# Performance work log

Measured on AMD Instinct MI355X. Metric: run time of the kernel, lower is better.

Reference implementation:

```python
import jax, jax.numpy as jnp
import numpy as np

B, S, HID = 1, 2048, 4096
NH, NKV, D = 32, 8, 128          # query heads, kv heads, head_dim
GROUPS = NH // NKV               # GQA repeat factor = 4
WINDOW = 1024                    # sliding-window size
ROPE_BASE = 10000.0


def setup_inputs() -> dict:
    key = jax.random.key(0)
    k = jax.random.split(key, 5)
    hidden_states = jax.random.normal(k[0], (B, S, HID), jnp.float32)
    Wq = jax.random.normal(k[1], (HID, HID), jnp.float32) * 0.02
    Wk = jax.random.normal(k[2], (NKV * D, HID), jnp.float32) * 0.02
    Wv = jax.random.normal(k[3], (NKV * D, HID), jnp.float32) * 0.02
    Wo = jax.random.normal(k[4], (HID, HID), jnp.float32) * 0.02
    position_ids = jnp.arange(S, dtype=jnp.int64 if jax.config.jax_enable_x64 else jnp.int32)[None, :]
    # Sliding-window causal additive mask [B,1,S,S]: key j visible to query i iff i-WINDOW < j <= i
    i = jnp.arange(S)
    visible = (i[None, :] <= i[:, None]) & (i[:, None] - i[None, :] < WINDOW)
    neg = jnp.finfo(jnp.float32).min
    attention_mask = jnp.where(visible, 0.0, neg)[None, None, :, :].astype(jnp.float32)
    return {"hidden_states": hidden_states, "attention_mask": attention_mask,
            "position_ids": position_ids, "Wq": Wq, "Wk": Wk, "Wv": Wv, "Wo": Wo}


def _rotate_half(x):
    x1, x2 = x[..., : D // 2], x[..., D // 2:]
    return jnp.concatenate((-x2, x1), axis=-1)


def _rope_cos_sin(position_ids, dtype):
    # inv_freq over even dims; gather-by-position_ids == direct indexing
    inv_freq = 1.0 / (ROPE_BASE ** (jnp.arange(0, D, 2, dtype=jnp.float32) / D))  # [D/2]
    freqs = position_ids.astype(jnp.float32)[..., None] * inv_freq                # [B,S,D/2]
    emb = jnp.concatenate((freqs, freqs), axis=-1)                                # [B,S,D]
    cos = jnp.cos(emb)[:, None, :, :].astype(dtype)                               # [B,1,S,D]
    sin = jnp.sin(emb)[:, None, :, :].astype(dtype)
    return cos, sin


def reference(hidden_states, attention_mask, position_ids, Wq, Wk, Wv, Wo):
    bsz, q_len, _ = hidden_states.shape
    # projections (nn.Linear: y = x @ W.T)
    q = (hidden_states @ Wq.T).reshape(bsz, q_len, NH, D).transpose(0, 2, 1, 3)    # [B,NH,S,D]
    k = (hidden_states @ Wk.T).reshape(bsz, q_len, NKV, D).transpose(0, 2, 1, 3)   # [B,NKV,S,D]
    v = (hidden_states @ Wv.T).reshape(bsz, q_len, NKV, D).transpose(0, 2, 1, 3)
    cos, sin = _rope_cos_sin(position_ids, q.dtype)
    q = q * cos + _rotate_half(q) * sin
    k = k * cos + _rotate_half(k) * sin
    # GQA repeat_kv (repeat_interleave along head dim)
    k = jnp.repeat(k, GROUPS, axis=1)                                              # [B,NH,S,D]
    v = jnp.repeat(v, GROUPS, axis=1)
    scores = jnp.einsum('bhqd,bhkd->bhqk', q, k) / np.sqrt(D)                       # [B,NH,S,S]
    scores = scores + attention_mask
    scores = jnp.maximum(scores, jnp.finfo(scores.dtype).min)
    probs = jax.nn.softmax(scores.astype(jnp.float32), axis=-1).astype(q.dtype)
    out = jnp.einsum('bhqk,bhkd->bhqd', probs, v)                                   # [B,NH,S,D]
    out = out.transpose(0, 2, 1, 3).reshape(bsz, q_len, HID)
    return out @ Wo.T
```

## Files before the change

### kernel.cpp

```cpp
#include <hip/hip_runtime.h>

#define S_LEN 2048
#define HID   4096
#define NH    32
#define NKV   8
#define DH    128
#define KVD   (NKV*DH)
#define WIN   1024
#define NTOT  6144

typedef __bf16 bf16_t;
typedef __bf16 bfrag  __attribute__((ext_vector_type(8)));
typedef __bf16 bf4    __attribute__((ext_vector_type(4)));
typedef float  ffrag  __attribute__((ext_vector_type(4)));
typedef float  f4     __attribute__((ext_vector_type(4)));

__global__ __launch_bounds__(256) void f32_to_bf16_kernel(const float* __restrict__ src,
                                                          bf16_t* __restrict__ dst, int n4) {
  int i = blockIdx.x * 256 + threadIdx.x;
  if (i < n4) {
    ffrag v = *(const ffrag*)(src + (size_t)i * 4);
    bf4 o;
    o[0] = (bf16_t)v[0]; o[1] = (bf16_t)v[1]; o[2] = (bf16_t)v[2]; o[3] = (bf16_t)v[3];
    *(bf4*)(dst + (size_t)i * 4) = o;
  }
}

__global__ __launch_bounds__(256) void cvt4_kernel(const float* __restrict__ h,
    const float* __restrict__ Wq, const float* __restrict__ Wk, const float* __restrict__ Wv,
    bf16_t* __restrict__ hB, bf16_t* __restrict__ WqB,
    bf16_t* __restrict__ WkB, bf16_t* __restrict__ WvB) {
  int i = blockIdx.x * 256 + threadIdx.x;
  const int N0 = S_LEN * HID / 4;
  const int N1 = N0 + HID * HID / 4;
  const int N2 = N1 + KVD * HID / 4;
  const float* s; bf16_t* d; int off;
  if (i < N0)      { s = h;  d = hB;  off = i; }
  else if (i < N1) { s = Wq; d = WqB; off = i - N0; }
  else if (i < N2) { s = Wk; d = WkB; off = i - N1; }
  else             { s = Wv; d = WvB; off = i - N2; }
  ffrag v = *(const ffrag*)(s + (size_t)off * 4);
  bf4 o;
  o[0] = (bf16_t)v[0]; o[1] = (bf16_t)v[1]; o[2] = (bf16_t)v[2]; o[3] = (bf16_t)v[3];
  *(bf4*)(d + (size_t)off * 4) = o;
}


__device__ __forceinline__ void load_lds16(const bf16_t* g, bf16_t* l) {
  __builtin_amdgcn_global_load_lds((__attribute__((address_space(1))) void*)g,
                                   (__attribute__((address_space(3))) void*)l,
                                   16, 0, 0);
}

#define BARW() asm volatile("s_barrier" ::: "memory")
#define WAITV(n) asm volatile("s_waitcnt vmcnt(" #n ")" ::: "memory")

template <int BNR, int OUT_MODE>
__device__ __forceinline__ void gemm_body(const bf16_t* __restrict__ A,
                                          const bf16_t* __restrict__ B,
                                          void* __restrict__ Cv,
                                          int N, bf16_t* lds) {
  constexpr int K     = 4096;
  constexpr int NT    = K / 32;
  constexpr int NTF   = BNR / 64;
  constexpr int WCOLS = BNR / 4;
  constexpr int ABUFE = 4096;
  constexpr int BBUFE = BNR * 32;

  bf16_t* Asb = lds;
  bf16_t* Bsb = lds + 4 * ABUFE;

  const int raw  = blockIdx.x;
  const int xcd  = raw & 7;
  const int slot = raw >> 3;
  const int bx   = xcd * 4 + (slot & 3);
  const int by   = slot >> 2;
  const int row0 = by * 128;
  const int col0 = bx * BNR;

  const int tid  = threadIdx.x;
  const int wave = tid >> 6;
  const int lane = tid & 63;
  const int wr = wave >> 2, wc = wave & 3;
  const int n = lane & 15, qd = lane >> 4;

  const int rsub = tid >> 2;
  const int sg   = (tid & 3) ^ (rsub & 3);
  const bf16_t* Ag  = A + (size_t)(row0 + rsub) * K + sg * 8;
  const bf16_t* Bg  = B + (size_t)(col0 + rsub) * K + sg * 8;
  const bf16_t* Bg2 = B + (size_t)(col0 + 128 + rsub) * K + sg * 8;
  const int wbase = wave * 512;

  const int lsw = n * 32 + (qd ^ (n & 3)) * 8;

  ffrag acc[4][NTF];
#pragma unroll
  for (int mt = 0; mt < 4; ++mt)
#pragma unroll
    for (int nt = 0; nt < NTF; ++nt) {
      acc[mt][nt][0] = 0.f; acc[mt][nt][1] = 0.f; acc[mt][nt][2] = 0.f; acc[mt][nt][3] = 0.f;
    }

  auto STAGE = [&](int t, int b) {
    const int ko = t * 32;
    load_lds16(Ag + ko, Asb + b * ABUFE + wbase);
    load_lds16(Bg + ko, Bsb + b * BBUFE + wbase);
    if constexpr (BNR == 192) {
      if (tid < 256) load_lds16(Bg2 + ko, Bsb + b * BBUFE + 4096 + wbase);
    }
  };

  STAGE(0, 0); STAGE(1, 1); STAGE(2, 2);
  if constexpr (BNR == 192) { if (wave < 4) { WAITV(6); } else { WAITV(4); } }
  else { WAITV(4); }
  BARW();

  for (int t = 0; t < NT; ++t) {
    const int b = t & 3;
    if (t + 3 < NT) STAGE(t + 3, (t + 3) & 3);

    const bf16_t* pa = Asb + b * ABUFE + wr * 2048 + lsw;
    const bf16_t* pb = Bsb + b * BBUFE + wc * (WCOLS * 32) + lsw;
    bfrag av[4], bv[NTF];
#pragma unroll
    for (int mt = 0; mt < 4; ++mt) av[mt] = *(const bfrag*)(pa + mt * 512);
#pragma unroll
    for (int nt = 0; nt < NTF; ++nt) bv[nt] = *(const bfrag*)(pb + nt * 512);

    __builtin_amdgcn_s_setprio(1);
#pragma unroll
    for (int mt = 0; mt < 4; ++mt)
#pragma unroll
      for (int nt = 0; nt < NTF; ++nt)
        acc[mt][nt] = __builtin_amdgcn_mfma_f32_16x16x32_bf16(av[mt], bv[nt], acc[mt][nt], 0, 0, 0);
    __builtin_amdgcn_s_setprio(0);

    if (t + 1 < NT) {
      if (t + 3 < NT) {
        if constexpr (BNR == 192) { if (wave < 4) { WAITV(6); } else { WAITV(4); } }
        else { WAITV(4); }
      } else if (t + 2 < NT) {
        if constexpr (BNR == 192) { if (wave < 4) { WAITV(3); } else { WAITV(2); } }
        else { WAITV(2); }
      } else {
        WAITV(0);
      }
      BARW();
    }
  }

  const int orow = row0 + wr * 64 + qd * 4;
  const int ocol = col0 + wc * WCOLS + n;
#pragma unroll
  for (int mt = 0; mt < 4; ++mt)
#pragma unroll
    for (int nt = 0; nt < NTF; ++nt)
#pragma unroll
      for (int r = 0; r < 4; ++r) {
        size_t idx = (size_t)(orow + mt * 16 + r) * N + (ocol + nt * 16);
        if (OUT_MODE == 1) ((bf16_t*)Cv)[idx] = (bf16_t)acc[mt][nt][r];
        else               ((float*)Cv)[idx]  = acc[mt][nt][r];
      }
}

__global__ __launch_bounds__(512, 4) void gemm_qkv_kernel(const bf16_t* __restrict__ hB,
                                                          const bf16_t* __restrict__ Wqkv,
                                                          bf16_t* __restrict__ C) {
  __shared__ __align__(16) bf16_t lds[4 * 4096 + 4 * 6144];
  gemm_body<192, 1>(hB, Wqkv, C, NTOT, lds);
}

__global__ __launch_bounds__(512, 4) void gemm_out_kernel(const bf16_t* __restrict__ A,
                                                          const bf16_t* __restrict__ B,
                                                          float* __restrict__ out) {
  __shared__ __align__(16) bf16_t lds[4 * 4096 + 4 * 4096];
  gemm_body<128, 0>(A, B, out, HID, lds);
}

__global__ __launch_bounds__(256) void ropecvt_kernel(const bf16_t* __restrict__ Cqkv,
                                                      bf16_t* __restrict__ Qb,
                                                      bf16_t* __restrict__ Kb,
                                                      bf16_t* __restrict__ Vb) {
  int idx = blockIdx.x * 256 + threadIdx.x;
  int g  = idx & 7;
  int t  = idx >> 3;
  int hh = t % 48;
  int s  = t / 48;
  const bf16_t* r0 = Cqkv + (size_t)s * NTOT + hh * 128;
  bfrag a0 = *(const bfrag*)&r0[g * 8];
  bfrag a1 = *(const bfrag*)&r0[g * 8 + 64];
  bf16_t* p;
  bool rope;
  if (hh < NH)           { p = Qb + (size_t)s * HID + hh * DH;        rope = true; }
  else if (hh < NH+NKV)  { p = Kb + (size_t)s * KVD + (hh - NH) * DH; rope = true; }
  else                   { p = Vb + (size_t)s * KVD + (hh - 40) * DH; rope = false; }
  bfrag o1, o2;
#pragma unroll
  for (int j = 0; j < 8; ++j) {
    float x1 = (float)a0[j];
    float x2 = (float)a1[j];
    if (rope) {
      int d = g * 8 + j;
      float inv = exp2f((float)d * (-13.287712379549449f / 64.f));
      float ang = (float)s * inv;
      float sn = sinf(ang), cs = cosf(ang);
      o1[j] = (bf16_t)(x1 * cs - x2 * sn);
      o2[j] = (bf16_t)(x2 * cs + x1 * sn);
    } else {
      o1[j] = (bf16_t)x1;
      o2[j] = (bf16_t)x2;
    }
  }
  *(bfrag*)&p[g * 8]      = o1;
  *(bfrag*)&p[g * 8 + 64] = o2;
}

#define KS_STRIDE 136
#define VT_STRIDE 72
#define PS_STRIDE 72

__global__ __launch_bounds__(256, 3) void attn_kernel(const bf16_t* __restrict__ Q,
                                                      const bf16_t* __restrict__ Kc,
                                                      const bf16_t* __restrict__ Vc,
                                                      bf16_t* __restrict__ AO) {
  const int qt   = 31 - blockIdx.x;
  const int h    = blockIdx.y;
  const int kvh  = h >> 2;
  const int q0   = qt * 64;
  const int tid  = threadIdx.x;
  const int wq   = tid >> 6;
  const int lane = tid & 63;
  const int n    = lane & 15;
  const int quad = lane >> 4;
  const float scale = 0.08838834764831845f;

  __shared__ __align__(16) bf16_t Ks[64 * KS_STRIDE];
  __shared__ __align__(16) bf16_t VT[128 * VT_STRIDE];
  __shared__ __align__(16) bf16_t Ps[4][16 * PS_STRIDE];

  bfrag aq[4];
#pragma unroll
  for (int kc = 0; kc < 4; ++kc) {
    bfrag t = *(const bfrag*)&Q[(size_t)(q0 + wq * 16 + n) * HID + h * DH + kc * 32 + quad * 8];
#pragma unroll
    for (int e = 0; e < 8; ++e) t[e] = (bf16_t)((float)t[e] * scale);
    aq[kc] = t;
  }

  ffrag acc[8];
#pragma unroll
  for (int dt = 0; dt < 8; ++dt) { acc[dt][0] = 0.f; acc[dt][1] = 0.f; acc[dt][2] = 0.f; acc[dt][3] = 0.f; }
  float lrow[4] = {0.f, 0.f, 0.f, 0.f};

  const int ktlo = (q0 >= WIN) ? ((q0 - (WIN - 1)) >> 6) : 0;
  const int kthi = (q0 + 63) >> 6;

  const int kg = tid & 15;
  const int dg = tid >> 4;

  bfrag pk[4], pv[4];
  {
    const int k0 = ktlo * 64;
#pragma unroll
    for (int i = 0; i < 4; ++i) {
      int pos = i * 256 + tid;
      pk[i] = *(const bfrag*)&Kc[(size_t)(k0 + (pos >> 4)) * KVD + kvh * DH + (pos & 15) * 8];
    }
#pragma unroll
    for (int j = 0; j < 4; ++j)
      pv[j] = *(const bfrag*)&Vc[(size_t)(k0 + j * 16 + kg) * KVD + kvh * DH + dg * 8];
  }

  for (int kt = ktlo; kt <= kthi; ++kt) {
    const int k0 = kt * 64;
    __syncthreads();
#pragma unroll
    for (int i = 0; i < 4; ++i) {
      int pos = i * 256 + tid;
      *(bfrag*)&Ks[(pos >> 4) * KS_STRIDE + (pos & 15) * 8] = pk[i];
    }
#pragma unroll
    for (int i = 0; i < 8; ++i) {
      bf4 pkk;
      pkk[0] = pv[0][i]; pkk[1] = pv[1][i]; pkk[2] = pv[2][i]; pkk[3] = pv[3][i];
      *(bf4*)&VT[(dg * 8 + i) * VT_STRIDE + kg * 4] = pkk;
    }
    __syncthreads();
    if (kt < kthi) {
      const int k1 = k0 + 64;
#pragma unroll
      for (int i = 0; i < 4; ++i) {
        int pos = i * 256 + tid;
        pk[i] = *(const bfrag*)&Kc[(size_t)(k1 + (pos >> 4)) * KVD + kvh * DH + (pos & 15) * 8];
      }
#pragma unroll
      for (int j = 0; j < 4; ++j)
        pv[j] = *(const bfrag*)&Vc[(size_t)(k1 + j * 16 + kg) * KVD + kvh * DH + dg * 8];
    }

    ffrag s[4];
#pragma unroll
    for (int nt = 0; nt < 4; ++nt) { s[nt][0] = 0.f; s[nt][1] = 0.f; s[nt][2] = 0.f; s[nt][3] = 0.f; }
#pragma unroll
    for (int kc = 0; kc < 4; ++kc) {
      bfrag bk[4];
#pragma unroll
      for (int nt = 0; nt < 4; ++nt)
        bk[nt] = *(const bfrag*)&Ks[(nt * 16 + n) * KS_STRIDE + kc * 32 + quad * 8];
#pragma unroll
      for (int nt = 0; nt < 4; ++nt)
        s[nt] = __builtin_amdgcn_mfma_f32_16x16x32_bf16(aq[kc], bk[nt], s[nt], 0, 0, 0);
    }

    const bool full = (k0 + 63 <= q0) && (q0 + 63 - k0 < WIN);
    if (!full) {
#pragma unroll
      for (int nt = 0; nt < 4; ++nt)
#pragma unroll
        for (int r = 0; r < 4; ++r) {
          int q = q0 + wq * 16 + quad * 4 + r;
          int k = k0 + nt * 16 + n;
          bool vis = (k <= q) && ((q - k) < WIN);
          if (!vis) s[nt][r] = -1e30f;
        }
    }

#pragma unroll
    for (int r = 0; r < 4; ++r) {
      bf4 pkk;
      float ps0 = __expf(s[0][r]);
      float ps1 = __expf(s[1][r]);
      float ps2 = __expf(s[2][r]);
      float ps3 = __expf(s[3][r]);
      lrow[r] += (ps0 + ps1) + (ps2 + ps3);
      pkk[0] = (bf16_t)ps0; pkk[1] = (bf16_t)ps1; pkk[2] = (bf16_t)ps2; pkk[3] = (bf16_t)ps3;
      *(bf4*)&Ps[wq][(quad * 4 + r) * PS_STRIDE + n * 4] = pkk;
    }

#pragma unroll
    for (int kc = 0; kc < 2; ++kc) {
      bfrag ap = *(const bfrag*)&Ps[wq][n * PS_STRIDE + kc * 32 + quad * 8];
#pragma unroll
      for (int dt = 0; dt < 8; ++dt) {
        bfrag bv = *(const bfrag*)&VT[(dt * 16 + n) * VT_STRIDE + kc * 32 + quad * 8];
        acc[dt] = __builtin_amdgcn_mfma_f32_16x16x32_bf16(ap, bv, acc[dt], 0, 0, 0);
      }
    }
  }

#pragma unroll
  for (int off = 1; off < 16; off <<= 1)
#pragma unroll
    for (int r = 0; r < 4; ++r) lrow[r] += __shfl_xor(lrow[r], off);
  float inv[4];
#pragma unroll
  for (int r = 0; r < 4; ++r) inv[r] = 1.f / lrow[r];
#pragma unroll
  for (int dt = 0; dt < 8; ++dt)
#pragma unroll
    for (int r = 0; r < 4; ++r)
      AO[(size_t)(q0 + wq * 16 + quad * 4 + r) * HID + h * DH + dt * 16 + n] =
          (bf16_t)(acc[dt][r] * inv[r]);
}

extern "C" void kernel_launch(void* const* d_in, const int* in_sizes, int n_in,
                              void* d_out, int out_size, void* d_ws, size_t ws_size,
                              hipStream_t stream) {
  const float* h  = (const float*)d_in[0];
  const float* Wq = (const float*)d_in[3];
  const float* Wk = (const float*)d_in[4];
  const float* Wv = (const float*)d_in[5];
  const float* Wo = (const float*)d_in[6];
  float* out = (float*)d_out;

  char* ws = (char*)d_ws;
  const size_t MB = (size_t)1 << 20;
  bf16_t* hB    = (bf16_t*)(ws + 0 * MB);
  bf16_t* Qb    = (bf16_t*)(ws + 0 * MB);
  bf16_t* WqB   = (bf16_t*)(ws + 16 * MB);
  bf16_t* WkB   = (bf16_t*)(ws + 48 * MB);
  bf16_t* WvB   = (bf16_t*)(ws + 56 * MB);
  bf16_t* Cqkv  = (bf16_t*)(ws + 64 * MB);
  bf16_t* WoB   = (bf16_t*)(ws + 64 * MB);
  bf16_t* AOb   = (bf16_t*)(ws + 96 * MB);
  bf16_t* Kb    = (bf16_t*)(ws + 112 * MB);
  bf16_t* Vb    = (bf16_t*)(ws + 116 * MB);

  cvt4_kernel<<<(S_LEN * HID + HID * HID + 2 * KVD * HID) / 4 / 256, 256, 0, stream>>>(
      h, Wq, Wk, Wv, hB, WqB, WkB, WvB);

  gemm_qkv_kernel<<<512, 512, 0, stream>>>(hB, WqB, Cqkv);

  ropecvt_kernel<<<(S_LEN * 48 * 8) / 256, 256, 0, stream>>>(Cqkv, Qb, Kb, Vb);

  f32_to_bf16_kernel<<<(HID * HID / 4 + 255) / 256, 256, 0, stream>>>(Wo, WoB, HID * HID / 4);

  attn_kernel<<<dim3(32, NH), 256, 0, stream>>>(Qb, Kb, Vb, AOb);

  gemm_out_kernel<<<512, 512, 0, stream>>>(AOb, WoB, out);
}
```

Measured before the change: 475.9 us.

## Switch GEMM mainloop to BK=64 double-buffered LDS with 8-way swizzle

```diff
diff --git a/kernel.cpp b/kernel.cpp
--- a/kernel.cpp
+++ b/kernel.cpp
@@ -54,6 +54,8 @@
 
 #define BARW() asm volatile("s_barrier" ::: "memory")
 #define WAITV(n) asm volatile("s_waitcnt vmcnt(" #n ")" ::: "memory")
+#define LGKM0() do { asm volatile("s_waitcnt lgkmcnt(0)" ::: "memory"); \
+                     __builtin_amdgcn_sched_barrier(0); } while (0)
 
 template <int BNR, int OUT_MODE>
 __device__ __forceinline__ void gemm_body(const bf16_t* __restrict__ A,
@@ -61,14 +63,14 @@
                                           void* __restrict__ Cv,
                                           int N, bf16_t* lds) {
   constexpr int K     = 4096;
-  constexpr int NT    = K / 32;
+  constexpr int NT    = K / 64;
   constexpr int NTF   = BNR / 64;
-  constexpr int WCOLS = BNR / 4;
-  constexpr int ABUFE = 4096;
-  constexpr int BBUFE = BNR * 32;
-
-  bf16_t* Asb = lds;
-  bf16_t* Bsb = lds + 4 * ABUFE;
+  constexpr int WC    = BNR / 4;
+  constexpr int ABUFE = 128 * 64;
+  constexpr int BBUFE = BNR * 64;
+
+  bf16_t* As0 = lds;
+  bf16_t* Bs0 = lds + 2 * ABUFE;
 
   const int raw  = blockIdx.x;
   const int xcd  = raw & 7;
@@ -84,14 +86,16 @@
   const int wr = wave >> 2, wc = wave & 3;
   const int n = lane & 15, qd = lane >> 4;
 
-  const int rsub = tid >> 2;
-  const int sg   = (tid & 3) ^ (rsub & 3);
-  const bf16_t* Ag  = A + (size_t)(row0 + rsub) * K + sg * 8;
-  const bf16_t* Bg  = B + (size_t)(col0 + rsub) * K + sg * 8;
-  const bf16_t* Bg2 = B + (size_t)(col0 + 128 + rsub) * K + sg * 8;
+  const int rsub = tid >> 3;
+  const int sg   = (tid & 7) ^ (rsub & 7);
+  const bf16_t* Ag = A + (size_t)(row0 + rsub) * K + sg * 8;
+  const bf16_t* Bg = B + (size_t)(col0 + rsub) * K + sg * 8;
   const int wbase = wave * 512;
 
-  const int lsw = n * 32 + (qd ^ (n & 3)) * 8;
+  const int pg0 = ( qd      ^ (n & 7)) * 8;
+  const int pg1 = ((4 | qd) ^ (n & 7)) * 8;
+  const int abase = (wr * 64 + n) * 64;
+  const int bbase = (wc * WC + n) * 64;
 
   ffrag acc[4][NTF];
 #pragma unroll
@@ -101,32 +105,31 @@
       acc[mt][nt][0] = 0.f; acc[mt][nt][1] = 0.f; acc[mt][nt][2] = 0.f; acc[mt][nt][3] = 0.f;
     }
 
-  auto STAGE = [&](int t, int b) {
-    const int ko = t * 32;
-    load_lds16(Ag + ko, Asb + b * ABUFE + wbase);
-    load_lds16(Bg + ko, Bsb + b * BBUFE + wbase);
-    if constexpr (BNR == 192) {
-      if (tid < 256) load_lds16(Bg2 + ko, Bsb + b * BBUFE + 4096 + wbase);
-    }
+  auto STAGE = [&](int t, int s) {
+    const int ko = t * 64;
+    bf16_t* as = As0 + s * ABUFE + wbase;
+    bf16_t* bs = Bs0 + s * BBUFE + wbase;
+    load_lds16(Ag + ko, as);
+    load_lds16(Ag + (size_t)64 * K + ko, as + 4096);
+    load_lds16(Bg + ko, bs);
+    load_lds16(Bg + (size_t)64 * K + ko, bs + 4096);
+    if constexpr (BNR == 192) load_lds16(Bg + (size_t)128 * K + ko, bs + 8192);
   };
 
-  STAGE(0, 0); STAGE(1, 1); STAGE(2, 2);
-  if constexpr (BNR == 192) { if (wave < 4) { WAITV(6); } else { WAITV(4); } }
-  else { WAITV(4); }
+  STAGE(0, 0); STAGE(1, 1);
+  if constexpr (BNR == 192) { WAITV(5); } else { WAITV(4); }
   BARW();
 
   for (int t = 0; t < NT; ++t) {
-    const int b = t & 3;
-    if (t + 3 < NT) STAGE(t + 3, (t + 3) & 3);
-
-    const bf16_t* pa = Asb + b * ABUFE + wr * 2048 + lsw;
-    const bf16_t* pb = Bsb + b * BBUFE + wc * (WCOLS * 32) + lsw;
+    const int s = t & 1;
+    const bf16_t* Asl = As0 + s * ABUFE;
+    const bf16_t* Bsl = Bs0 + s * BBUFE;
     bfrag av[4], bv[NTF];
-#pragma unroll
-    for (int mt = 0; mt < 4; ++mt) av[mt] = *(const bfrag*)(pa + mt * 512);
-#pragma unroll
-    for (int nt = 0; nt < NTF; ++nt) bv[nt] = *(const bfrag*)(pb + nt * 512);
-
+
+#pragma unroll
+    for (int mt = 0; mt < 4; ++mt) av[mt] = *(const bfrag*)(Asl + abase + mt * 1024 + pg0);
+#pragma unroll
+    for (int nt = 0; nt < NTF; ++nt) bv[nt] = *(const bfrag*)(Bsl + bbase + nt * 1024 + pg0);
     __builtin_amdgcn_s_setprio(1);
 #pragma unroll
     for (int mt = 0; mt < 4; ++mt)
@@ -135,22 +138,30 @@
         acc[mt][nt] = __builtin_amdgcn_mfma_f32_16x16x32_bf16(av[mt], bv[nt], acc[mt][nt], 0, 0, 0);
     __builtin_amdgcn_s_setprio(0);
 
+#pragma unroll
+    for (int mt = 0; mt < 4; ++mt) av[mt] = *(const bfrag*)(Asl + abase + mt * 1024 + pg1);
+#pragma unroll
+    for (int nt = 0; nt < NTF; ++nt) bv[nt] = *(const bfrag*)(Bsl + bbase + nt * 1024 + pg1);
+    __builtin_amdgcn_s_setprio(1);
+#pragma unroll
+    for (int mt = 0; mt < 4; ++mt)
+#pragma unroll
+      for (int nt = 0; nt < NTF; ++nt)
+        acc[mt][nt] = __builtin_amdgcn_mfma_f32_16x16x32_bf16(av[mt], bv[nt], acc[mt][nt], 0, 0, 0);
+    __builtin_amdgcn_s_setprio(0);
+
+    LGKM0();
+    BARW();
+    if (t + 2 < NT) STAGE(t + 2, s);
     if (t + 1 < NT) {
-      if (t + 3 < NT) {
-        if constexpr (BNR == 192) { if (wave < 4) { WAITV(6); } else { WAITV(4); } }
-        else { WAITV(4); }
-      } else if (t + 2 < NT) {
-        if constexpr (BNR == 192) { if (wave < 4) { WAITV(3); } else { WAITV(2); } }
-        else { WAITV(2); }
-      } else {
-        WAITV(0);
-      }
+      if (t + 2 < NT) { if constexpr (BNR == 192) { WAITV(5); } else { WAITV(4); } }
+      else            { WAITV(0); }
       BARW();
     }
   }
 
   const int orow = row0 + wr * 64 + qd * 4;
-  const int ocol = col0 + wc * WCOLS + n;
+  const int ocol = col0 + wc * WC + n;
 #pragma unroll
   for (int mt = 0; mt < 4; ++mt)
 #pragma unroll
@@ -166,14 +177,14 @@
 __global__ __launch_bounds__(512, 4) void gemm_qkv_kernel(const bf16_t* __restrict__ hB,
                                                           const bf16_t* __restrict__ Wqkv,
                                                           bf16_t* __restrict__ C) {
-  __shared__ __align__(16) bf16_t lds[4 * 4096 + 4 * 6144];
+  __shared__ __align__(16) bf16_t lds[2 * 128 * 64 + 2 * 192 * 64];
   gemm_body<192, 1>(hB, Wqkv, C, NTOT, lds);
 }
 
 __global__ __launch_bounds__(512, 4) void gemm_out_kernel(const bf16_t* __restrict__ A,
                                                           const bf16_t* __restrict__ B,
                                                           float* __restrict__ out) {
-  __shared__ __align__(16) bf16_t lds[4 * 4096 + 4 * 4096];
+  __shared__ __align__(16) bf16_t lds[2 * 128 * 64 + 2 * 128 * 64];
   gemm_body<128, 0>(A, B, out, HID, lds);
 }
 
```

Measured after the change: 454.4 us. -4.5%, faster.
